# Performance work log

Hardware: AMD Instinct MI355X
Metric: run time of the kernel (lower is better)

The kernel has to match this reference:

```python
import jax, jax.numpy as jnp
import numpy as np

B, NUM_CAMS, C, N_ANCHOR = 1, 6, 256, 900
NUM_LEVELS, NUM_FIXED, NUM_LEARN, NUM_GROUPS = 4, 7, 6, 8
NUM_PTS = NUM_FIXED + NUM_LEARN
IMG_W, IMG_H = 704, 256
SHAPES = [(64, 176), (32, 88), (16, 44), (8, 22)]  # strides 4,8,16,32


def setup_inputs() -> dict:
    key = jax.random.key(0)
    ks = jax.random.split(key, 12)
    sum_hw = sum(h * w for h, w in SHAPES)
    feature = jax.random.normal(ks[0], (B, NUM_CAMS, sum_hw, C), jnp.float32)
    spatial_shapes = jnp.array(SHAPES, dtype=jnp.int32)
    starts = np.cumsum([0] + [h * w for h, w in SHAPES[:-1]])
    level_start_index = jnp.array(starts, dtype=jnp.int32)
    # anchor: [x,y,z, log(w),log(l),log(h), sin(yaw), cos(yaw), vx,vy,vz]
    center = jax.random.uniform(ks[1], (B, N_ANCHOR, 3), minval=-40.0, maxval=40.0) * jnp.array([1.0, 1.0, 0.05])
    size = jnp.log(jnp.array([2.0, 4.5, 1.7])) * jnp.ones((B, N_ANCHOR, 3))
    yaw = jax.random.uniform(ks[2], (B, N_ANCHOR, 1), minval=-np.pi, maxval=np.pi)
    anchor = jnp.concatenate([center, size, jnp.sin(yaw), jnp.cos(yaw), jnp.zeros((B, N_ANCHOR, 3))], axis=-1).astype(jnp.float32)
    instance_feature = jax.random.normal(ks[3], (B, N_ANCHOR, C), jnp.float32)
    time_interval = jnp.full((B,), 0.5, jnp.float32)
    # plausible lidar2img = K @ [R|t] for 6 surround cameras
    l2i = []
    for c in range(NUM_CAMS):
        a = 2.0 * np.pi * c / NUM_CAMS
        Rz = np.array([[np.cos(a), -np.sin(a), 0.0], [np.sin(a), np.cos(a), 0.0], [0.0, 0.0, 1.0]])
        swap = np.array([[0.0, -1.0, 0.0], [0.0, 0.0, -1.0], [1.0, 0.0, 0.0]])  # lidar axes -> camera axes
        Rcam = swap @ Rz.T
        t = -Rcam @ np.array([0.0, 0.0, 1.5])
        E = np.eye(4); E[:3, :3] = Rcam; E[:3, 3] = t
        K = np.eye(4); K[0, 0] = K[1, 1] = 400.0; K[0, 2] = IMG_W / 2.0; K[1, 2] = IMG_H / 2.0
        l2i.append(K @ E)
    lidar2img = jnp.asarray(np.broadcast_to(np.stack(l2i)[None], (B, NUM_CAMS, 4, 4)), jnp.float32)
    image_wh = jnp.broadcast_to(jnp.array([IMG_W, IMG_H], jnp.float32), (B, NUM_CAMS, 2))
    s = 0.02
    n_w = NUM_CAMS * NUM_LEVELS * NUM_PTS * NUM_GROUPS
    return dict(
        instance_feature=instance_feature, anchor=anchor, time_interval=time_interval,
        feature=feature, spatial_shapes=spatial_shapes, level_start_index=level_start_index,
        lidar2img=lidar2img, image_wh=image_wh,
        enc_w=jax.random.normal(ks[4], (11, C)) * s, enc_b=jnp.zeros((C,), jnp.float32),
        kp_fixed=jax.random.normal(ks[5], (NUM_FIXED, 3)) * 0.5,
        kp_w=jax.random.normal(ks[6], (C, NUM_LEARN * 3)) * s, kp_b=jnp.zeros((NUM_LEARN * 3,), jnp.float32),
        wfc_w=jax.random.normal(ks[7], (C, n_w)) * s, wfc_b=jnp.zeros((n_w,), jnp.float32),
        out_w=jax.random.normal(ks[8], (C, C)) * s, out_b=jnp.zeros((C,), jnp.float32),
    )


def _bilinear_sample(feature, spatial_shapes, level_start_index, pts, valid):
    # feature: [B,Cm,sumHW,C]; pts: [B,Cm,N,P,2] normalized to [0,1]; valid: [B,Cm,N,P]
    Bn, Cm, _, Cd = feature.shape
    N, P = pts.shape[2], pts.shape[3]
    per_level = []
    for l in range(NUM_LEVELS):
        H = spatial_shapes[l, 0]
        W = spatial_shapes[l, 1]
        start = level_start_index[l]
        # grid_sample align_corners=False convention
        x = pts[..., 0] * W - 0.5
        y = pts[..., 1] * H - 0.5
        x0f = jnp.floor(x); y0f = jnp.floor(y)
        wx = (x - x0f)[..., None]
        wy = (y - y0f)[..., None]
        x0 = x0f.astype(jnp.int32); y0 = y0f.astype(jnp.int32)

        def gather(xi, yi):
            ok = (xi >= 0) & (xi < W) & (yi >= 0) & (yi < H) & valid
            xi_c = jnp.clip(xi, 0, W - 1)
            yi_c = jnp.clip(yi, 0, H - 1)
            idx = (start + yi_c * W + xi_c).reshape(Bn, Cm, N * P, 1)
            g = jnp.take_along_axis(feature, idx, axis=2).reshape(Bn, Cm, N, P, Cd)
            return g * ok[..., None]

        v = (gather(x0, y0) * (1 - wx) * (1 - wy)
             + gather(x0 + 1, y0) * wx * (1 - wy)
             + gather(x0, y0 + 1) * (1 - wx) * wy
             + gather(x0 + 1, y0 + 1) * wx * wy)
        per_level.append(v)
    return jnp.stack(per_level, axis=4)  # [B,Cm,N,P,L,C]


def _forward(instance_feature, anchor, feature, spatial_shapes, level_start_index,
             lidar2img, image_wh, enc_w, enc_b, kp_fixed, kp_w, kp_b, wfc_w, wfc_b, out_w, out_b):
    Bn, N, Cd = instance_feature.shape
    anchor_embed = anchor @ enc_w + enc_b                      # anchor_encoder
    # --- keypoint generation (7 fixed + 6 learnable), scaled by box size, rotated by yaw ---
    center = anchor[..., :3]
    size = jnp.exp(anchor[..., 3:6])
    sin_y, cos_y = anchor[..., 6:7], anchor[..., 7:8]
    learn = (instance_feature @ kp_w + kp_b).reshape(Bn, N, NUM_LEARN, 3)
    offs = jnp.concatenate([jnp.broadcast_to(kp_fixed, (Bn, N, NUM_FIXED, 3)), learn], axis=2)
    offs = offs * size[:, :, None, :]
    ox, oy, oz = offs[..., 0], offs[..., 1], offs[..., 2]
    rx = cos_y * ox - sin_y * oy
    ry = sin_y * ox + cos_y * oy
    kp = jnp.stack([rx, ry, oz], axis=-1) + center[:, :, None, :]          # [B,N,P,3]
    # --- project to each camera ---
    kp_h = jnp.concatenate([kp, jnp.ones_like(kp[..., :1])], axis=-1)
    p = jnp.einsum('bcij,bnpj->bcnpi', lidar2img, kp_h)                    # [B,Cm,N,P,4]
    depth = p[..., 2]
    xy = p[..., :2] / jnp.clip(depth, 1e-5, None)[..., None]
    pts = xy / image_wh[:, :, None, None, :]                               # [0,1] normalized
    valid = depth > 1e-5
    # --- multi-scale multi-camera bilinear gather ---
    feats = _bilinear_sample(feature, spatial_shapes, level_start_index, pts, valid)  # [B,Cm,N,P,L,C]
    # --- group-wise attention weights, softmax over cams*levels*pts ---
    w = ((instance_feature + anchor_embed) @ wfc_w + wfc_b).reshape(Bn, N, -1, NUM_GROUPS)
    w = jax.nn.softmax(w, axis=-2).reshape(Bn, N, NUM_CAMS, NUM_LEVELS, NUM_PTS, NUM_GROUPS)
    f = jnp.transpose(feats, (0, 2, 1, 4, 3, 5)).reshape(
        Bn, N, NUM_CAMS, NUM_LEVELS, NUM_PTS, NUM_GROUPS, Cd // NUM_GROUPS)
    agg = jnp.sum(f * w[..., None], axis=(2, 3, 4)).reshape(Bn, N, Cd)
    return instance_feature + (agg @ out_w + out_b)


def reference(instance_feature, anchor, time_interval, feature, spatial_shapes, level_start_index,
              lidar2img, image_wh, enc_w, enc_b, kp_fixed, kp_w, kp_b, wfc_w, wfc_b, out_w, out_b):
    # time_interval is only consumed by the 'refine' op, which is not in the executed op list
    return _forward(instance_feature, anchor, feature, spatial_shapes, level_start_index,
                    lidar2img, image_wh, enc_w, enc_b, kp_fixed, kp_w, kp_b, wfc_w, wfc_b, out_w, out_b)
```

## Files before the change

### kernel.cpp

```cpp
#include <hip/hip_runtime.h>
#include <math.h>

#define N_ANCHOR   900
#define NUM_CAMS   6
#define CDIM       256
#define NUM_LEVELS 4
#define NUM_FIXED  7
#define NUM_LEARN  6
#define NUM_PTS    13
#define NUM_GROUPS 8
#define NW         2496
#define NI         312
#define SUM_HW     14960

__global__ __launch_bounds__(256) void k_prep(
    const float* __restrict__ inst, const float* __restrict__ anchor,
    const float* __restrict__ l2i, const float* __restrict__ image_wh,
    const float* __restrict__ kp_fixed, const float* __restrict__ kp_w,
    const float* __restrict__ kp_b,
    const float* __restrict__ enc_w, const float* __restrict__ enc_b,
    float* __restrict__ q, float* __restrict__ pts_out,
    float* __restrict__ valid_out) {
  const int n = blockIdx.x;
  const int t = threadIdx.x;
  __shared__ float anc[11];
  __shared__ float learn[NUM_LEARN * 3];
  __shared__ float kps[NUM_PTS][3];
  __shared__ float ins[CDIM];

  const float iv = inst[n * CDIM + t];
  ins[t] = iv;
  if (t < 11) anc[t] = anchor[n * 11 + t];
  __syncthreads();

  {
    float s = enc_b[t] + iv;
    #pragma unroll
    for (int k = 0; k < 11; ++k) s += anc[k] * enc_w[k * CDIM + t];
    q[n * CDIM + t] = s;
  }

  if (t < NUM_LEARN * 3) {
    float s = kp_b[t];
    for (int k = 0; k < CDIM; ++k) s += ins[k] * kp_w[k * (NUM_LEARN * 3) + t];
    learn[t] = s;
  }
  __syncthreads();

  if (t < NUM_PTS) {
    const float sx = expf(anc[3]), sy = expf(anc[4]), sz = expf(anc[5]);
    float ox, oy, oz;
    if (t < NUM_FIXED) {
      ox = kp_fixed[t * 3 + 0]; oy = kp_fixed[t * 3 + 1]; oz = kp_fixed[t * 3 + 2];
    } else {
      const int j = (t - NUM_FIXED) * 3;
      ox = learn[j + 0]; oy = learn[j + 1]; oz = learn[j + 2];
    }
    ox *= sx; oy *= sy; oz *= sz;
    const float sn = anc[6], cs = anc[7];
    kps[t][0] = cs * ox - sn * oy + anc[0];
    kps[t][1] = sn * ox + cs * oy + anc[1];
    kps[t][2] = oz + anc[2];
  }
  __syncthreads();

  if (t < NUM_CAMS * NUM_PTS) {
    const int cam = t / NUM_PTS, p = t % NUM_PTS;
    const float* M = l2i + cam * 16;
    const float kx = kps[p][0], ky = kps[p][1], kz = kps[p][2];
    const float px = M[0] * kx + M[1] * ky + M[2]  * kz + M[3];
    const float py = M[4] * kx + M[5] * ky + M[6]  * kz + M[7];
    const float pz = M[8] * kx + M[9] * ky + M[10] * kz + M[11];
    const float d = fmaxf(pz, 1e-5f);
    const float u = (px / d) / image_wh[cam * 2 + 0];
    const float v = (py / d) / image_wh[cam * 2 + 1];
    const int o = n * NUM_CAMS * NUM_PTS + t;
    pts_out[o * 2 + 0] = u;
    pts_out[o * 2 + 1] = v;
    valid_out[o] = (pz > 1e-5f) ? 1.0f : 0.0f;
  }
}

__global__ __launch_bounds__(256) void k_wgemm(
    const float* __restrict__ q, const float* __restrict__ wfc_w,
    const float* __restrict__ wfc_b, float* __restrict__ raw) {
  const int tid = threadIdx.x;
  const int n0 = blockIdx.x * 64;
  const int m0 = blockIdx.y * 64;
  const int tx = tid & 15, ty = tid >> 4;
  const int ar = tid >> 2, av4 = tid & 3;
  const int br = tid >> 4, bc4 = (tid & 15) * 4;
  __shared__ float AsT[16][68];
  __shared__ float Bs[16][64];
  float acc[4][4] = {{0.f}};

  const int arow = m0 + ar;
  for (int k0 = 0; k0 < CDIM; k0 += 16) {
    float4 a4 = make_float4(0.f, 0.f, 0.f, 0.f);
    if (arow < N_ANCHOR) a4 = *(const float4*)&q[arow * CDIM + k0 + av4 * 4];
    const float4 b4 = *(const float4*)&wfc_w[(size_t)(k0 + br) * NW + n0 + bc4];
    AsT[av4 * 4 + 0][ar] = a4.x;
    AsT[av4 * 4 + 1][ar] = a4.y;
    AsT[av4 * 4 + 2][ar] = a4.z;
    AsT[av4 * 4 + 3][ar] = a4.w;
    *(float4*)&Bs[br][bc4] = b4;
    __syncthreads();
    #pragma unroll
    for (int kk = 0; kk < 16; ++kk) {
      const float4 av = *(const float4*)&AsT[kk][ty * 4];
      const float4 bv = *(const float4*)&Bs[kk][tx * 4];
      acc[0][0] += av.x * bv.x; acc[0][1] += av.x * bv.y;
      acc[0][2] += av.x * bv.z; acc[0][3] += av.x * bv.w;
      acc[1][0] += av.y * bv.x; acc[1][1] += av.y * bv.y;
      acc[1][2] += av.y * bv.z; acc[1][3] += av.y * bv.w;
      acc[2][0] += av.z * bv.x; acc[2][1] += av.z * bv.y;
      acc[2][2] += av.z * bv.z; acc[2][3] += av.z * bv.w;
      acc[3][0] += av.w * bv.x; acc[3][1] += av.w * bv.y;
      acc[3][2] += av.w * bv.z; acc[3][3] += av.w * bv.w;
    }
    __syncthreads();
  }

  const int col = n0 + tx * 4;
  const float4 bias = *(const float4*)&wfc_b[col];
  #pragma unroll
  for (int i = 0; i < 4; ++i) {
    const int row = m0 + ty * 4 + i;
    if (row < N_ANCHOR) {
      float4 o;
      o.x = acc[i][0] + bias.x; o.y = acc[i][1] + bias.y;
      o.z = acc[i][2] + bias.z; o.w = acc[i][3] + bias.w;
      *(float4*)&raw[(size_t)row * NW + col] = o;
    }
  }
}

__global__ __launch_bounds__(256) void k_smstats(
    const float* __restrict__ raw, float* __restrict__ stats) {
  const int n = blockIdx.x, t = threadIdx.x;
  __shared__ float row_s[NW];
  const float4* src = (const float4*)(raw + (size_t)n * NW);
  for (int j = t; j < NW / 4; j += 256)
    *(float4*)&row_s[j * 4] = src[j];
  __syncthreads();
  const int g = t >> 5, lane = t & 31;
  float m = -1e30f;
  for (int i = lane; i < NI; i += 32) m = fmaxf(m, row_s[i * NUM_GROUPS + g]);
  #pragma unroll
  for (int o = 16; o > 0; o >>= 1) m = fmaxf(m, __shfl_down(m, o, 32));
  m = __shfl(m, 0, 32);
  float s = 0.0f;
  for (int i = lane; i < NI; i += 32) s += expf(row_s[i * NUM_GROUPS + g] - m);
  #pragma unroll
  for (int o = 16; o > 0; o >>= 1) s += __shfl_down(s, o, 32);
  if (lane == 0) {
    stats[n * 16 + g] = m;
    stats[n * 16 + 8 + g] = 1.0f / s;
  }
}

__global__ __launch_bounds__(256) void k_sample(
    const float* __restrict__ feature,
    const int* __restrict__ spatial_shapes, const int* __restrict__ level_start,
    const float* __restrict__ pts, const float* __restrict__ valid,
    const float* __restrict__ raw, const float* __restrict__ stats,
    float* __restrict__ agg) {
  const int n = blockIdx.x;
  const int cam = blockIdx.y;
  const int t = threadIdx.x;
  const int q = t >> 6;
  const int ci = t & 63;
  const int g = ci >> 3;
  __shared__ float w_s[NUM_LEVELS * NUM_PTS * NUM_GROUPS];
  __shared__ float uv_s[NUM_PTS][2];
  __shared__ float val_s[NUM_PTS];
  __shared__ float mx_s[NUM_GROUPS], inv_s[NUM_GROUPS];
  __shared__ int shp[NUM_LEVELS][2];
  __shared__ int lst[NUM_LEVELS];
  __shared__ int any_valid;
  __shared__ float4 red[256];

  if (t < NUM_PTS) {
    const int o = (n * NUM_CAMS + cam) * NUM_PTS + t;
    uv_s[t][0] = pts[o * 2 + 0];
    uv_s[t][1] = pts[o * 2 + 1];
    val_s[t] = valid[o];
  }
  if (t < NUM_GROUPS) {
    mx_s[t]  = stats[n * 16 + t];
    inv_s[t] = stats[n * 16 + 8 + t];
  }
  if (t < NUM_LEVELS) {
    shp[t][0] = spatial_shapes[t * 2 + 0];
    shp[t][1] = spatial_shapes[t * 2 + 1];
    lst[t] = level_start[t];
  }
  if (t == 0) any_valid = 0;
  __syncthreads();
  if (t < NUM_PTS && val_s[t] != 0.0f) any_valid = 1;
  __syncthreads();

  float* aout = agg + ((size_t)n * NUM_CAMS + cam) * CDIM;
  if (!any_valid) {
    if (t < 64) *(float4*)&aout[t * 4] = make_float4(0.f, 0.f, 0.f, 0.f);
    return;
  }

  for (int j = t; j < 416; j += 256)
    w_s[j] = expf(raw[(size_t)n * NW + cam * 416 + j] - mx_s[j & 7]) * inv_s[j & 7];
  __syncthreads();

  const int dx = q & 1, dy = q >> 1;
  float4 acc = make_float4(0.f, 0.f, 0.f, 0.f);
  const float* fcam = feature + (size_t)cam * SUM_HW * CDIM;
  for (int p = 0; p < NUM_PTS; ++p) {
    if (val_s[p] == 0.0f) continue;
    const float u = uv_s[p][0], v = uv_s[p][1];
    #pragma unroll
    for (int l = 0; l < NUM_LEVELS; ++l) {
      const int H = shp[l][0], W = shp[l][1], st = lst[l];
      const float x = u * (float)W - 0.5f;
      const float y = v * (float)H - 0.5f;
      const float x0f = floorf(x), y0f = floorf(y);
      const float wx = x - x0f, wy = y - y0f;
      const int xx = (int)x0f + dx;
      const int yy = (int)y0f + dy;
      if (xx >= 0 && xx < W && yy >= 0 && yy < H) {
        const float cw = w_s[(l * NUM_PTS + p) * 8 + g]
                       * (dx ? wx : 1.0f - wx) * (dy ? wy : 1.0f - wy);
        const float4 f = *(const float4*)&fcam[(size_t)(st + yy * W + xx) * CDIM + ci * 4];
        acc.x += cw * f.x; acc.y += cw * f.y;
        acc.z += cw * f.z; acc.w += cw * f.w;
      }
    }
  }
  red[t] = acc;
  __syncthreads();
  if (t < 64) {
    float4 s = red[t];
    const float4 b1 = red[t + 64], b2 = red[t + 128], b3 = red[t + 192];
    s.x += b1.x + b2.x + b3.x;
    s.y += b1.y + b2.y + b3.y;
    s.z += b1.z + b2.z + b3.z;
    s.w += b1.w + b2.w + b3.w;
    *(float4*)&aout[t * 4] = s;
  }
}

__global__ __launch_bounds__(1024) void k_out(
    const float* __restrict__ inst, const float* __restrict__ agg,
    const float* __restrict__ out_w, const float* __restrict__ out_b,
    float* __restrict__ out) {
  const int n = blockIdx.x, t = threadIdx.x;
  const int col = t & 255, ks = t >> 8;
  __shared__ float a_s[CDIM];
  __shared__ float red[4][CDIM];

  if (t < CDIM) {
    float s = 0.0f;
    #pragma unroll
    for (int cam = 0; cam < NUM_CAMS; ++cam)
      s += agg[((size_t)n * NUM_CAMS + cam) * CDIM + t];
    a_s[t] = s;
  }
  __syncthreads();

  float partial = 0.0f;
  const int k0 = ks * 64;
  #pragma unroll
  for (int k = 0; k < 64; ++k)
    partial += a_s[k0 + k] * out_w[(k0 + k) * CDIM + col];
  red[ks][col] = partial;
  __syncthreads();

  if (t < CDIM) {
    const float s = red[0][t] + red[1][t] + red[2][t] + red[3][t];
    out[(size_t)n * CDIM + t] = s + out_b[t] + inst[(size_t)n * CDIM + t];
  }
}

extern "C" void kernel_launch(void* const* d_in, const int* in_sizes, int n_in,
                              void* d_out, int out_size, void* d_ws, size_t ws_size,
                              hipStream_t stream) {
  const float* inst           = (const float*)d_in[0];
  const float* anchor         = (const float*)d_in[1];
  const float* feature        = (const float*)d_in[3];
  const int*   spatial_shapes = (const int*)d_in[4];
  const int*   level_start    = (const int*)d_in[5];
  const float* l2i            = (const float*)d_in[6];
  const float* image_wh       = (const float*)d_in[7];
  const float* enc_w          = (const float*)d_in[8];
  const float* enc_b          = (const float*)d_in[9];
  const float* kp_fixed       = (const float*)d_in[10];
  const float* kp_w           = (const float*)d_in[11];
  const float* kp_b           = (const float*)d_in[12];
  const float* wfc_w          = (const float*)d_in[13];
  const float* wfc_b          = (const float*)d_in[14];
  const float* out_w          = (const float*)d_in[15];
  const float* out_b          = (const float*)d_in[16];

  float* ws    = (float*)d_ws;
  float* pts   = ws;
  float* valid = pts + N_ANCHOR * NUM_CAMS * NUM_PTS * 2;
  float* qbuf  = valid + N_ANCHOR * NUM_CAMS * NUM_PTS;
  float* wbuf  = qbuf + N_ANCHOR * CDIM;
  float* stats = wbuf + (size_t)N_ANCHOR * NW;
  float* agg   = stats + N_ANCHOR * 16;

  k_prep<<<N_ANCHOR, 256, 0, stream>>>(inst, anchor, l2i, image_wh,
                                       kp_fixed, kp_w, kp_b, enc_w, enc_b,
                                       qbuf, pts, valid);
  k_wgemm<<<dim3(NW / 64, (N_ANCHOR + 63) / 64), 256, 0, stream>>>(
      qbuf, wfc_w, wfc_b, wbuf);
  k_smstats<<<N_ANCHOR, 256, 0, stream>>>(wbuf, stats);
  k_sample<<<dim3(N_ANCHOR, NUM_CAMS), 256, 0, stream>>>(
      feature, spatial_shapes, level_start, pts, valid, wbuf, stats, agg);
  k_out<<<N_ANCHOR, 1024, 0, stream>>>(inst, agg, out_w, out_b, (float*)d_out);
}
```

Before: 244.7 us.

## Use bf16 MFMA for attention-weight GEMM with transposed bf16 weights

Stores the query in bf16 and adds a kernel that converts and transposes the wfc weight matrix to bf16. The FP32 SIMT 4x4 register-tile GEMM is replaced by an MFMA 16x16x32 bf16 kernel with an XOR-swizzled LDS tile for B. The goal is to cut the compute cost of the 900x2496x256 projection. The trade-offs are lower precision in the softmax logits and an extra kernel launch that converts the weights on every call.

```diff
diff --git a/kernel.cpp b/kernel.cpp
--- a/kernel.cpp
+++ b/kernel.cpp
@@ -13,13 +13,22 @@
 #define NI         312
 #define SUM_HW     14960
 
+typedef short short8 __attribute__((ext_vector_type(8)));
+typedef float floatx4 __attribute__((ext_vector_type(4)));
+
+__device__ __forceinline__ unsigned short f2bf(float x) {
+  unsigned u = __float_as_uint(x);
+  u += 0x7FFFu + ((u >> 16) & 1u);
+  return (unsigned short)(u >> 16);
+}
+
 __global__ __launch_bounds__(256) void k_prep(
     const float* __restrict__ inst, const float* __restrict__ anchor,
     const float* __restrict__ l2i, const float* __restrict__ image_wh,
     const float* __restrict__ kp_fixed, const float* __restrict__ kp_w,
     const float* __restrict__ kp_b,
     const float* __restrict__ enc_w, const float* __restrict__ enc_b,
-    float* __restrict__ q, float* __restrict__ pts_out,
+    unsigned short* __restrict__ qbf, float* __restrict__ pts_out,
     float* __restrict__ valid_out) {
   const int n = blockIdx.x;
   const int t = threadIdx.x;
@@ -37,7 +46,7 @@
     float s = enc_b[t] + iv;
     #pragma unroll
     for (int k = 0; k < 11; ++k) s += anc[k] * enc_w[k * CDIM + t];
-    q[n * CDIM + t] = s;
+    qbf[n * CDIM + t] = f2bf(s);
   }
 
   if (t < NUM_LEARN * 3) {
@@ -81,56 +90,88 @@
   }
 }
 
+__global__ __launch_bounds__(256) void k_cvtw(
+    const float* __restrict__ wfc_w, unsigned short* __restrict__ wbf_t) {
+  const int n0 = blockIdx.x * 64, k0 = blockIdx.y * 64;
+  const int t = threadIdx.x;
+  __shared__ float tile[64][65];
+  #pragma unroll
+  for (int i = 0; i < 4; ++i) {
+    const int kr = (t >> 4) + i * 16;
+    const int nc = (t & 15) * 4;
+    const float4 v = *(const float4*)&wfc_w[(size_t)(k0 + kr) * NW + n0 + nc];
+    tile[kr][nc + 0] = v.x; tile[kr][nc + 1] = v.y;
+    tile[kr][nc + 2] = v.z; tile[kr][nc + 3] = v.w;
+  }
+  __syncthreads();
+  #pragma unroll
+  for (int i = 0; i < 4; ++i) {
+    const int nr = (t >> 4) + i * 16;
+    const int kc = (t & 15) * 4;
+    ushort4 o;
+    o.x = f2bf(tile[kc + 0][nr]);
+    o.y = f2bf(tile[kc + 1][nr]);
+    o.z = f2bf(tile[kc + 2][nr]);
+    o.w = f2bf(tile[kc + 3][nr]);
+    *(ushort4*)&wbf_t[(size_t)(n0 + nr) * CDIM + k0 + kc] = o;
+  }
+}
+
 __global__ __launch_bounds__(256) void k_wgemm(
-    const float* __restrict__ q, const float* __restrict__ wfc_w,
+    const unsigned short* __restrict__ qbf,
+    const unsigned short* __restrict__ wbf_t,
     const float* __restrict__ wfc_b, float* __restrict__ raw) {
   const int tid = threadIdx.x;
+  const int w = tid >> 6;
+  const int l = tid & 63;
   const int n0 = blockIdx.x * 64;
   const int m0 = blockIdx.y * 64;
-  const int tx = tid & 15, ty = tid >> 4;
-  const int ar = tid >> 2, av4 = tid & 3;
-  const int br = tid >> 4, bc4 = (tid & 15) * 4;
-  __shared__ float AsT[16][68];
-  __shared__ float Bs[16][64];
-  float acc[4][4] = {{0.f}};
-
-  const int arow = m0 + ar;
-  for (int k0 = 0; k0 < CDIM; k0 += 16) {
-    float4 a4 = make_float4(0.f, 0.f, 0.f, 0.f);
-    if (arow < N_ANCHOR) a4 = *(const float4*)&q[arow * CDIM + k0 + av4 * 4];
-    const float4 b4 = *(const float4*)&wfc_w[(size_t)(k0 + br) * NW + n0 + bc4];
-    AsT[av4 * 4 + 0][ar] = a4.x;
-    AsT[av4 * 4 + 1][ar] = a4.y;
-    AsT[av4 * 4 + 2][ar] = a4.z;
-    AsT[av4 * 4 + 3][ar] = a4.w;
-    *(float4*)&Bs[br][bc4] = b4;
+  __shared__ unsigned short Bs[64 * 64];
+
+  floatx4 acc[4];
+  #pragma unroll
+  for (int s = 0; s < 4; ++s) acc[s] = (floatx4){0.f, 0.f, 0.f, 0.f};
+
+  const int arow = m0 + w * 16 + (l & 15);
+  const bool arow_ok = arow < N_ANCHOR;
+  const unsigned short* aptr = qbf + (size_t)arow * CDIM + (l >> 4) * 8;
+
+  for (int k0 = 0; k0 < CDIM; k0 += 64) {
+    #pragma unroll
+    for (int i = 0; i < 2; ++i) {
+      const int idx = tid + i * 256;
+      const int n = idx >> 3, kg = idx & 7;
+      const short8 bv =
+          *(const short8*)&wbf_t[(size_t)(n0 + n) * CDIM + k0 + kg * 8];
+      *(short8*)&Bs[n * 64 + ((kg ^ (n & 7)) * 8)] = bv;
+    }
     __syncthreads();
     #pragma unroll
-    for (int kk = 0; kk < 16; ++kk) {
-      const float4 av = *(const float4*)&AsT[kk][ty * 4];
-      const float4 bv = *(const float4*)&Bs[kk][tx * 4];
-      acc[0][0] += av.x * bv.x; acc[0][1] += av.x * bv.y;
-      acc[0][2] += av.x * bv.z; acc[0][3] += av.x * bv.w;
-      acc[1][0] += av.y * bv.x; acc[1][1] += av.y * bv.y;
-      acc[1][2] += av.y * bv.z; acc[1][3] += av.y * bv.w;
-      acc[2][0] += av.z * bv.x; acc[2][1] += av.z * bv.y;
-      acc[2][2] += av.z * bv.z; acc[2][3] += av.z * bv.w;
-      acc[3][0] += av.w * bv.x; acc[3][1] += av.w * bv.y;
-      acc[3][2] += av.w * bv.z; acc[3][3] += av.w * bv.w;
+    for (int c = 0; c < 2; ++c) {
+      short8 a = (short8){0, 0, 0, 0, 0, 0, 0, 0};
+      if (arow_ok) a = *(const short8*)&aptr[k0 + c * 32];
+      #pragma unroll
+      for (int s = 0; s < 4; ++s) {
+        const int nloc = s * 16 + (l & 15);
+        const int k8 = c * 4 + (l >> 4);
+        const short8 b = *(const short8*)&Bs[nloc * 64 + ((k8 ^ (nloc & 7)) * 8)];
+        acc[s] = __builtin_amdgcn_mfma_f32_16x16x32_bf16(a, b, acc[s], 0, 0, 0);
+      }
     }
     __syncthreads();
   }
 
-  const int col = n0 + tx * 4;
-  const float4 bias = *(const float4*)&wfc_b[col];
-  #pragma unroll
-  for (int i = 0; i < 4; ++i) {
-    const int row = m0 + ty * 4 + i;
-    if (row < N_ANCHOR) {
-      float4 o;
-      o.x = acc[i][0] + bias.x; o.y = acc[i][1] + bias.y;
-      o.z = acc[i][2] + bias.z; o.w = acc[i][3] + bias.w;
-      *(float4*)&raw[(size_t)row * NW + col] = o;
+  const int colb = n0 + (l & 15);
+  const int rowb = m0 + w * 16 + (l >> 4) * 4;
+  #pragma unroll
+  for (int s = 0; s < 4; ++s) {
+    const int col = colb + s * 16;
+    const float bias = wfc_b[col];
+    #pragma unroll
+    for (int r = 0; r < 4; ++r) {
+      const int row = rowb + r;
+      if (row < N_ANCHOR)
+        raw[(size_t)row * NW + col] = acc[s][r] + bias;
     }
   }
 }
@@ -302,16 +343,18 @@
   float* ws    = (float*)d_ws;
   float* pts   = ws;
   float* valid = pts + N_ANCHOR * NUM_CAMS * NUM_PTS * 2;
-  float* qbuf  = valid + N_ANCHOR * NUM_CAMS * NUM_PTS;
-  float* wbuf  = qbuf + N_ANCHOR * CDIM;
+  float* wbuf  = valid + N_ANCHOR * NUM_CAMS * NUM_PTS;
   float* stats = wbuf + (size_t)N_ANCHOR * NW;
   float* agg   = stats + N_ANCHOR * 16;
+  unsigned short* qbf   = (unsigned short*)(agg + N_ANCHOR * NUM_CAMS * CDIM);
+  unsigned short* wbf_t = qbf + N_ANCHOR * CDIM;
 
   k_prep<<<N_ANCHOR, 256, 0, stream>>>(inst, anchor, l2i, image_wh,
                                        kp_fixed, kp_w, kp_b, enc_w, enc_b,
-                                       qbuf, pts, valid);
+                                       qbf, pts, valid);
+  k_cvtw<<<dim3(NW / 64, CDIM / 64), 256, 0, stream>>>(wfc_w, wbf_t);
   k_wgemm<<<dim3(NW / 64, (N_ANCHOR + 63) / 64), 256, 0, stream>>>(
-      qbuf, wfc_w, wfc_b, wbuf);
+      qbf, wbf_t, wfc_b, wbuf);
   k_smstats<<<N_ANCHOR, 256, 0, stream>>>(wbuf, stats);
   k_sample<<<dim3(N_ANCHOR, NUM_CAMS), 256, 0, stream>>>(
       feature, spatial_shapes, level_start, pts, valid, wbuf, stats, agg);
```

Result: faster. 233.1 us (-4.7%).
